# Performance work log

Measured on AMD Instinct MI355X. Metric: run time of the kernel, lower is better.

Reference implementation:

```python
import jax, jax.numpy as jnp
import numpy as np

B, S, E, H = 4, 2048, 256, 8
D = E // H
SCALE = D ** -0.5


def setup_inputs() -> dict:
    key = jax.random.key(0)
    k1, k2, k3, k4, k5, k6 = jax.random.split(key, 6)
    x = jax.random.normal(k1, (B, S, E), dtype=jnp.float32)
    lengths = jax.random.randint(k2, (B,), S // 4, S + 1)
    # binary prefix mask, as assumed by mask[i].sum() == valid length in the original
    mask = (jnp.arange(S)[None, :] < lengths[:, None]).astype(jnp.int32)
    w_std = 1.0 / np.sqrt(E)
    Wq = jax.random.normal(k3, (E, E), dtype=jnp.float32) * w_std
    Wk = jax.random.normal(k4, (E, E), dtype=jnp.float32) * w_std
    Wv = jax.random.normal(k5, (E, E), dtype=jnp.float32) * w_std
    Wo = jax.random.normal(k6, (E, E), dtype=jnp.float32) * w_std
    return {"x": x, "mask": mask, "Wq": Wq, "Wk": Wk, "Wv": Wv, "Wo": Wo}


def _scramble_pad(attn_i, L):
    # attn_i: [S, H, D] attention output for one sample; only query rows < L are used.
    # Faithful to torch: attn[:L] viewed as [H, L, D] (after transpose(1,2)) then
    # reshape(L, E), zero-padded to [S, E]. The reshape mixes heads in a
    # length-dependent way, reproduced here with integer index arithmetic.
    L_safe = jnp.maximum(L, 1)
    flat = jnp.arange(S * E)                     # flat index into [H, L, D] row-major
    h = jnp.minimum(flat // (L_safe * D), H - 1)
    rem = flat % (L_safe * D)
    s = rem // D
    d = rem % D
    valid = flat < L * E
    vals = attn_i[s, h, d]
    return jnp.where(valid, vals, 0.0).reshape(S, E)


def reference(x, mask, Wq, Wk, Wv, Wo):
    # projections (torch Linear, no bias: y = x @ W.T), split heads
    Q = (x @ Wq.T).reshape(B, S, H, D)
    K = (x @ Wk.T).reshape(B, S, H, D)
    V = (x @ Wv.T).reshape(B, S, H, D)
    scores = jnp.einsum("bqhd,bkhd->bhqk", Q, K) * SCALE
    key_valid = mask[:, None, None, :] > 0       # prefix key mask == per-sample varlen attn
    scores = jnp.where(key_valid, scores, -1e30)
    P = jax.nn.softmax(scores, axis=-1)
    attn = jnp.einsum("bhqk,bkhd->bqhd", P, V)   # [B, S, H, D]
    lengths = mask.sum(axis=1)
    padded = jax.vmap(_scramble_pad)(attn, lengths)  # [B, S, E]
    return padded @ Wo.T
```

## Files before the change

### kernel.cpp

```cpp
#include <hip/hip_runtime.h>
#include <cmath>

#define Bn 4
#define Sn 2048
#define En 256
#define Hn 8
#define Dn 32
#define KD 256
#define NS 8
#define CHUNK 256

static constexpr float SCALE_F = 0.17677669529663687f;

typedef _Float16 half4_t __attribute__((ext_vector_type(4)));
typedef _Float16 half8_t __attribute__((ext_vector_type(8)));
typedef float float4_t __attribute__((ext_vector_type(4)));

__global__ __launch_bounds__(256) void len_kernel(const int* __restrict__ mask,
                                                  int* __restrict__ len) {
  int b = blockIdx.x, t = threadIdx.x;
  int s = 0;
  for (int i = t; i < Sn; i += 256) s += mask[b * Sn + i];
#pragma unroll
  for (int off = 32; off > 0; off >>= 1) s += __shfl_down(s, off, 64);
  __shared__ int red[4];
  if ((t & 63) == 0) red[t >> 6] = s;
  __syncthreads();
  if (t == 0) len[b] = red[0] + red[1] + red[2] + red[3];
}

__global__ __launch_bounds__(256) void cvt_kernel(
    const float* __restrict__ x, const float* __restrict__ Wq,
    const float* __restrict__ Wk, const float* __restrict__ Wv,
    const float* __restrict__ Wo, _Float16* __restrict__ xh,
    _Float16* __restrict__ Wh) {
  const size_t base = ((size_t)blockIdx.x * 256 + threadIdx.x) * 8;
  const float* src; _Float16* dst; size_t off;
  if (base < 2097152) { src = x; dst = xh; off = base; }
  else {
    size_t wi = base - 2097152;
    int w = (int)(wi >> 16);
    off = wi & 65535;
    src = (w == 0) ? Wq : (w == 1) ? Wk : (w == 2) ? Wv : Wo;
    dst = Wh + (size_t)w * 65536;
  }
  float4 a = *(const float4*)&src[off];
  float4 b2 = *(const float4*)&src[off + 4];
  half8_t h;
  h[0] = (_Float16)a.x;  h[1] = (_Float16)a.y;
  h[2] = (_Float16)a.z;  h[3] = (_Float16)a.w;
  h[4] = (_Float16)b2.x; h[5] = (_Float16)b2.y;
  h[6] = (_Float16)b2.z; h[7] = (_Float16)b2.w;
  *(half8_t*)&dst[off] = h;
}

__global__ __launch_bounds__(256) void qkv_gemm(
    const _Float16* __restrict__ xh, const _Float16* __restrict__ Wh,
    _Float16* __restrict__ Qh, _Float16* __restrict__ Kh,
    _Float16* __restrict__ Vt) {
  const int lane = threadIdx.x & 63;
  const int wv = threadIdx.x >> 6;
  const int quad = lane >> 4, l15 = lane & 15;
  const int n0 = blockIdx.x * 64;
  const int mw = blockIdx.y * 256 + wv * 64;

  float4_t C[4][4];
#pragma unroll
  for (int i = 0; i < 4; ++i)
#pragma unroll
    for (int j = 0; j < 4; ++j) C[i][j] = (float4_t){0.f, 0.f, 0.f, 0.f};

  for (int k0 = 0; k0 < KD; k0 += 32) {
    half8_t A[4], Bf[4];
#pragma unroll
    for (int i = 0; i < 4; ++i)
      A[i] = *(const half8_t*)&xh[(size_t)(mw + 16 * i + l15) * KD + k0 + quad * 8];
#pragma unroll
    for (int j = 0; j < 4; ++j)
      Bf[j] = *(const half8_t*)&Wh[(size_t)(n0 + 16 * j + l15) * KD + k0 + quad * 8];
#pragma unroll
    for (int i = 0; i < 4; ++i)
#pragma unroll
      for (int j = 0; j < 4; ++j)
        C[i][j] = __builtin_amdgcn_mfma_f32_16x16x32_f16(A[i], Bf[j], C[i][j], 0, 0, 0);
  }

  const int mat = n0 >> 8;
  if (mat < 2) {
    _Float16* dstH = mat ? Kh : Qh;
    const float scale = mat ? 1.0f : SCALE_F;
#pragma unroll
    for (int i = 0; i < 4; ++i)
#pragma unroll
      for (int j = 0; j < 4; ++j) {
        const int c = ((n0 + 16 * j) & 255) + l15;
        const int h = c >> 5, d = c & 31;
#pragma unroll
        for (int r = 0; r < 4; ++r) {
          const int m = mw + 16 * i + quad * 4 + r;
          const int b = m >> 11, s = m & (Sn - 1);
          dstH[((size_t)(b * Hn + h) * Sn + s) * Dn + d] =
              (_Float16)(C[i][j][r] * scale);
        }
      }
  } else {
#pragma unroll
    for (int i = 0; i < 4; ++i)
#pragma unroll
      for (int j = 0; j < 4; ++j) {
        const int c = ((n0 + 16 * j) & 255) + l15;
        const int h = c >> 5, d = c & 31;
        const int m = mw + 16 * i + quad * 4;
        const int b = m >> 11, s = m & (Sn - 1);
        half4_t hv;
#pragma unroll
        for (int r = 0; r < 4; ++r) hv[r] = (_Float16)C[i][j][r];
        *(half4_t*)&Vt[(size_t)(b * Hn + h) * (Sn * Dn) +
                       (size_t)(s >> 5) * 1024 + d * 32 + (s & 31)] = hv;
      }
  }
}

__global__ __launch_bounds__(256) void out_gemm(
    const _Float16* __restrict__ Ph, const _Float16* __restrict__ Woh,
    float* __restrict__ out) {
  const int lane = threadIdx.x & 63;
  const int wv = threadIdx.x >> 6;
  const int quad = lane >> 4, l15 = lane & 15;
  const int n0 = blockIdx.x * 64;
  const int mw = blockIdx.y * 256 + wv * 64;

  float4_t C[4][4];
#pragma unroll
  for (int i = 0; i < 4; ++i)
#pragma unroll
    for (int j = 0; j < 4; ++j) C[i][j] = (float4_t){0.f, 0.f, 0.f, 0.f};

  for (int k0 = 0; k0 < KD; k0 += 32) {
    half8_t A[4], Bf[4];
#pragma unroll
    for (int i = 0; i < 4; ++i)
      A[i] = *(const half8_t*)&Ph[(size_t)(mw + 16 * i + l15) * KD + k0 + quad * 8];
#pragma unroll
    for (int j = 0; j < 4; ++j)
      Bf[j] = *(const half8_t*)&Woh[(size_t)(n0 + 16 * j + l15) * KD + k0 + quad * 8];
#pragma unroll
    for (int i = 0; i < 4; ++i)
#pragma unroll
      for (int j = 0; j < 4; ++j)
        C[i][j] = __builtin_amdgcn_mfma_f32_16x16x32_f16(A[i], Bf[j], C[i][j], 0, 0, 0);
  }

#pragma unroll
  for (int i = 0; i < 4; ++i)
#pragma unroll
    for (int j = 0; j < 4; ++j)
#pragma unroll
      for (int r = 0; r < 4; ++r)
        out[(size_t)(mw + 16 * i + quad * 4 + r) * En + n0 + 16 * j + l15] =
            C[i][j][r];
}

__global__ __launch_bounds__(256) void attn_kernel(
    const _Float16* __restrict__ Qh, const _Float16* __restrict__ Kh,
    const _Float16* __restrict__ Vt, const int* __restrict__ len,
    float* __restrict__ pacc, float* __restrict__ pl) {
  const int split = blockIdx.x & (NS - 1);
  const int qg = blockIdx.x >> 3;
  const int h = blockIdx.y, b = blockIdx.z;
  const int L = len[b];
  const int lane = threadIdx.x & 63;
  const int wv = threadIdx.x >> 6;
  const int q0 = (qg * 4 + wv) * 64;
  if (q0 >= L) return;
  const int ks = split * CHUNK;
  if (ks >= L) return;
  const int ke = min(L, ks + CHUNK);

  const int quad = lane >> 4;
  const int l15 = lane & 15;
  const size_t bh = (size_t)(b * Hn + h) * Sn;
  const _Float16* Vt0 = &Vt[(size_t)(b * Hn + h) * (Sn * Dn)];

  half8_t qf[4];
#pragma unroll
  for (int t = 0; t < 4; ++t)
    qf[t] = *(const half8_t*)&Qh[(bh + q0 + 16 * t + l15) * Dn + quad * 8];

  float4_t o0[4], o1[4];
  float ll[4];
#pragma unroll
  for (int t = 0; t < 4; ++t) {
    o0[t] = (float4_t){0.f, 0.f, 0.f, 0.f};
    o1[t] = (float4_t){0.f, 0.f, 0.f, 0.f};
    ll[t] = 0.f;
  }

  const int vo0 = l15 * 32 + quad * 4;
  const int vo1 = (l15 + 16) * 32 + quad * 4;

  const _Float16* vt_c = &Vt0[(size_t)(ks >> 5) * 1024];
  half8_t kfc0 = *(const half8_t*)&Kh[(bh + ks + l15) * Dn + quad * 8];
  half8_t kfc1 = *(const half8_t*)&Kh[(bh + ks + 16 + l15) * Dn + quad * 8];
  half4_t v0c = *(const half4_t*)&vt_c[vo0];
  half4_t v1c = *(const half4_t*)&vt_c[vo1];
  half4_t v2c = *(const half4_t*)&vt_c[vo0 + 16];
  half4_t v3c = *(const half4_t*)&vt_c[vo1 + 16];

  for (int k0 = ks; k0 < ke; k0 += 32) {
    const int kn = (k0 + 32 < ke) ? k0 + 32 : ks;
    const _Float16* vt_n = &Vt0[(size_t)(kn >> 5) * 1024];
    const half8_t kfn0 = *(const half8_t*)&Kh[(bh + kn + l15) * Dn + quad * 8];
    const half8_t kfn1 = *(const half8_t*)&Kh[(bh + kn + 16 + l15) * Dn + quad * 8];
    const half4_t v0n = *(const half4_t*)&vt_n[vo0];
    const half4_t v1n = *(const half4_t*)&vt_n[vo1];
    const half4_t v2n = *(const half4_t*)&vt_n[vo0 + 16];
    const half4_t v3n = *(const half4_t*)&vt_n[vo1 + 16];

    float4_t st0[4], st1[4];
#pragma unroll
    for (int t = 0; t < 4; ++t) {
      st0[t] = (float4_t){0.f, 0.f, 0.f, 0.f};
      st1[t] = (float4_t){0.f, 0.f, 0.f, 0.f};
      st0[t] = __builtin_amdgcn_mfma_f32_16x16x32_f16(kfc0, qf[t], st0[t], 0, 0, 0);
      st1[t] = __builtin_amdgcn_mfma_f32_16x16x32_f16(kfc1, qf[t], st1[t], 0, 0, 0);
    }
    const int ka = k0 + quad * 4, kb = k0 + 16 + quad * 4;
#pragma unroll
    for (int t = 0; t < 4; ++t) {
      half4_t pf0, pf1;
#pragma unroll
      for (int r = 0; r < 4; ++r) {
        const float pa = __expf((ka + r < ke) ? st0[t][r] : -3.0e38f);
        const float pb = __expf((kb + r < ke) ? st1[t][r] : -3.0e38f);
        ll[t] += pa + pb;
        pf0[r] = (_Float16)pa;
        pf1[r] = (_Float16)pb;
      }
      o0[t] = __builtin_amdgcn_mfma_f32_16x16x16f16(pf0, v0c, o0[t], 0, 0, 0);
      o1[t] = __builtin_amdgcn_mfma_f32_16x16x16f16(pf0, v1c, o1[t], 0, 0, 0);
      o0[t] = __builtin_amdgcn_mfma_f32_16x16x16f16(pf1, v2c, o0[t], 0, 0, 0);
      o1[t] = __builtin_amdgcn_mfma_f32_16x16x16f16(pf1, v3c, o1[t], 0, 0, 0);
    }
    kfc0 = kfn0; kfc1 = kfn1;
    v0c = v0n; v1c = v1n; v2c = v2n; v3c = v3n;
  }

#pragma unroll
  for (int t = 0; t < 4; ++t) {
    ll[t] += __shfl_xor(ll[t], 16);
    ll[t] += __shfl_xor(ll[t], 32);
  }

  const size_t idx0 = ((size_t)(b * Hn + h) * NS + split) * Sn + q0;
#pragma unroll
  for (int t = 0; t < 4; ++t) {
#pragma unroll
    for (int r = 0; r < 4; ++r) {
      float* pp = &pacc[(idx0 + 16 * t + quad * 4 + r) * 32];
      pp[l15] = o0[t][r];
      pp[l15 + 16] = o1[t][r];
    }
  }
  if (quad == 0) {
#pragma unroll
    for (int t = 0; t < 4; ++t) pl[idx0 + 16 * t + l15] = ll[t];
  }
}

__global__ __launch_bounds__(256) void combine_kernel(const float* __restrict__ pacc,
                                                      const float* __restrict__ pl,
                                                      const int* __restrict__ len,
                                                      _Float16* __restrict__ Ph) {
  const int b = blockIdx.z;
  const int L = len[b];
  if (blockIdx.y == Hn) {
    _Float16* base = Ph + (size_t)b * Sn * En;
    const size_t end = (size_t)Sn * En;
    const size_t stride = (size_t)gridDim.x * 256 * 8;
    half8_t z = {0, 0, 0, 0, 0, 0, 0, 0};
    for (size_t idx = (size_t)L * En + ((size_t)blockIdx.x * 256 + threadIdx.x) * 8;
         idx < end; idx += stride)
      *(half8_t*)&base[idx] = z;
    return;
  }
  const int h = blockIdx.y;
  const int q = blockIdx.x * 256 + threadIdx.x;
  if (q >= L) return;
  const size_t base = (size_t)(b * Hn + h) * NS * Sn;

  float T = 0.f;
  float o[32];
#pragma unroll
  for (int d = 0; d < 32; ++d) o[d] = 0.f;
#pragma unroll
  for (int sp = 0; sp < NS; ++sp) {
    if (sp * CHUNK < L) {
      T += pl[base + (size_t)sp * Sn + q];
      const float4* pp = (const float4*)&pacc[(base + (size_t)sp * Sn + q) * 32];
#pragma unroll
      for (int i = 0; i < 8; ++i) {
        float4 v = pp[i];
        o[i * 4 + 0] += v.x;
        o[i * 4 + 1] += v.y;
        o[i * 4 + 2] += v.z;
        o[i * 4 + 3] += v.w;
      }
    }
  }
  const float inv = 1.0f / T;
  _Float16* dst = &Ph[(size_t)b * Sn * En + (size_t)h * L * Dn + (size_t)q * Dn];
#pragma unroll
  for (int i = 0; i < 4; ++i) {
    half8_t hv;
#pragma unroll
    for (int t2 = 0; t2 < 8; ++t2) hv[t2] = (_Float16)(o[i * 8 + t2] * inv);
    *(half8_t*)&dst[i * 8] = hv;
  }
}

extern "C" void kernel_launch(void* const* d_in, const int* in_sizes, int n_in,
                              void* d_out, int out_size, void* d_ws, size_t ws_size,
                              hipStream_t stream) {
  (void)in_sizes; (void)n_in; (void)out_size; (void)ws_size;
  const float* x  = (const float*)d_in[0];
  const int* mask = (const int*)d_in[1];
  const float* Wq = (const float*)d_in[2];
  const float* Wk = (const float*)d_in[3];
  const float* Wv = (const float*)d_in[4];
  const float* Wo = (const float*)d_in[5];
  float* out = (float*)d_out;

  float* wsf = (float*)d_ws;
  int* lengths = (int*)d_ws;
  const size_t BHSD = (size_t)Bn * Hn * Sn * Dn;
  _Float16* xh = (_Float16*)(wsf + 64);
  _Float16* Wh = xh + BHSD;
  _Float16* Qh = Wh + 4 * 65536;
  _Float16* Kh = Qh + BHSD;
  _Float16* Vt = Kh + BHSD;
  _Float16* Ph = Vt + BHSD;
  float* pacc = (float*)(Ph + BHSD);
  float* pl = pacc + (size_t)Bn * Hn * NS * Sn * 32;

  len_kernel<<<dim3(Bn), 256, 0, stream>>>(mask, lengths);
  cvt_kernel<<<dim3((2097152 + 262144) / (256 * 8)), 256, 0, stream>>>(
      x, Wq, Wk, Wv, Wo, xh, Wh);
  qkv_gemm<<<dim3(12, 32), 256, 0, stream>>>(xh, Wh, Qh, Kh, Vt);
  attn_kernel<<<dim3((Sn / 256) * NS, Hn, Bn), 256, 0, stream>>>(
      Qh, Kh, Vt, lengths, pacc, pl);
  combine_kernel<<<dim3(Sn / 256, Hn + 1, Bn), 256, 0, stream>>>(
      pacc, pl, lengths, Ph);
  out_gemm<<<dim3(4, 32), 256, 0, stream>>>(Ph, Wh + 3 * 65536, out);
}
```

Measured before the change: 154.5 us.

## Double KV splits, store fp16 partials, and skip masking on full key tiles

Doubles the number of key splits in the split-K attention, from 8 chunks of 256 keys to 16 chunks of 128, which gives more blocks and less serial work per block. To keep the partial-accumulator traffic bounded, partial outputs are now stored as fp16 instead of fp32, and the combine kernel reads half8 vectors. The softmax loop gets a fast path with no length masking for full 32-key tiles. The costs are twice as many partials to combine and lower precision in the partial sums, since values are unnormalized exps rounded to fp16.

```diff
diff --git a/kernel.cpp b/kernel.cpp
--- a/kernel.cpp
+++ b/kernel.cpp
@@ -7,8 +7,8 @@
 #define Hn 8
 #define Dn 32
 #define KD 256
-#define NS 8
-#define CHUNK 256
+#define NS 16
+#define CHUNK 128
 
 static constexpr float SCALE_F = 0.17677669529663687f;
 
@@ -164,9 +164,9 @@
 __global__ __launch_bounds__(256) void attn_kernel(
     const _Float16* __restrict__ Qh, const _Float16* __restrict__ Kh,
     const _Float16* __restrict__ Vt, const int* __restrict__ len,
-    float* __restrict__ pacc, float* __restrict__ pl) {
+    _Float16* __restrict__ pacc, float* __restrict__ pl) {
   const int split = blockIdx.x & (NS - 1);
-  const int qg = blockIdx.x >> 3;
+  const int qg = blockIdx.x >> 4;
   const int h = blockIdx.y, b = blockIdx.z;
   const int L = len[b];
   const int lane = threadIdx.x & 63;
@@ -225,22 +225,42 @@
       st0[t] = __builtin_amdgcn_mfma_f32_16x16x32_f16(kfc0, qf[t], st0[t], 0, 0, 0);
       st1[t] = __builtin_amdgcn_mfma_f32_16x16x32_f16(kfc1, qf[t], st1[t], 0, 0, 0);
     }
-    const int ka = k0 + quad * 4, kb = k0 + 16 + quad * 4;
-#pragma unroll
-    for (int t = 0; t < 4; ++t) {
-      half4_t pf0, pf1;
-#pragma unroll
-      for (int r = 0; r < 4; ++r) {
-        const float pa = __expf((ka + r < ke) ? st0[t][r] : -3.0e38f);
-        const float pb = __expf((kb + r < ke) ? st1[t][r] : -3.0e38f);
-        ll[t] += pa + pb;
-        pf0[r] = (_Float16)pa;
-        pf1[r] = (_Float16)pb;
-      }
-      o0[t] = __builtin_amdgcn_mfma_f32_16x16x16f16(pf0, v0c, o0[t], 0, 0, 0);
-      o1[t] = __builtin_amdgcn_mfma_f32_16x16x16f16(pf0, v1c, o1[t], 0, 0, 0);
-      o0[t] = __builtin_amdgcn_mfma_f32_16x16x16f16(pf1, v2c, o0[t], 0, 0, 0);
-      o1[t] = __builtin_amdgcn_mfma_f32_16x16x16f16(pf1, v3c, o1[t], 0, 0, 0);
+
+    if (k0 + 32 <= ke) {
+#pragma unroll
+      for (int t = 0; t < 4; ++t) {
+        half4_t pf0, pf1;
+#pragma unroll
+        for (int r = 0; r < 4; ++r) {
+          const float pa = __expf(st0[t][r]);
+          const float pb = __expf(st1[t][r]);
+          ll[t] += pa + pb;
+          pf0[r] = (_Float16)pa;
+          pf1[r] = (_Float16)pb;
+        }
+        o0[t] = __builtin_amdgcn_mfma_f32_16x16x16f16(pf0, v0c, o0[t], 0, 0, 0);
+        o1[t] = __builtin_amdgcn_mfma_f32_16x16x16f16(pf0, v1c, o1[t], 0, 0, 0);
+        o0[t] = __builtin_amdgcn_mfma_f32_16x16x16f16(pf1, v2c, o0[t], 0, 0, 0);
+        o1[t] = __builtin_amdgcn_mfma_f32_16x16x16f16(pf1, v3c, o1[t], 0, 0, 0);
+      }
+    } else {
+      const int ka = k0 + quad * 4, kb = k0 + 16 + quad * 4;
+#pragma unroll
+      for (int t = 0; t < 4; ++t) {
+        half4_t pf0, pf1;
+#pragma unroll
+        for (int r = 0; r < 4; ++r) {
+          const float pa = __expf((ka + r < ke) ? st0[t][r] : -3.0e38f);
+          const float pb = __expf((kb + r < ke) ? st1[t][r] : -3.0e38f);
+          ll[t] += pa + pb;
+          pf0[r] = (_Float16)pa;
+          pf1[r] = (_Float16)pb;
+        }
+        o0[t] = __builtin_amdgcn_mfma_f32_16x16x16f16(pf0, v0c, o0[t], 0, 0, 0);
+        o1[t] = __builtin_amdgcn_mfma_f32_16x16x16f16(pf0, v1c, o1[t], 0, 0, 0);
+        o0[t] = __builtin_amdgcn_mfma_f32_16x16x16f16(pf1, v2c, o0[t], 0, 0, 0);
+        o1[t] = __builtin_amdgcn_mfma_f32_16x16x16f16(pf1, v3c, o1[t], 0, 0, 0);
+      }
     }
     kfc0 = kfn0; kfc1 = kfn1;
     v0c = v0n; v1c = v1n; v2c = v2n; v3c = v3n;
@@ -257,9 +277,9 @@
   for (int t = 0; t < 4; ++t) {
 #pragma unroll
     for (int r = 0; r < 4; ++r) {
-      float* pp = &pacc[(idx0 + 16 * t + quad * 4 + r) * 32];
-      pp[l15] = o0[t][r];
-      pp[l15 + 16] = o1[t][r];
+      _Float16* pp = &pacc[(idx0 + 16 * t + quad * 4 + r) * 32];
+      pp[l15] = (_Float16)o0[t][r];
+      pp[l15 + 16] = (_Float16)o1[t][r];
     }
   }
   if (quad == 0) {
@@ -268,7 +288,7 @@
   }
 }
 
-__global__ __launch_bounds__(256) void combine_kernel(const float* __restrict__ pacc,
+__global__ __launch_bounds__(256) void combine_kernel(const _Float16* __restrict__ pacc,
                                                       const float* __restrict__ pl,
                                                       const int* __restrict__ len,
                                                       _Float16* __restrict__ Ph) {
@@ -297,14 +317,12 @@
   for (int sp = 0; sp < NS; ++sp) {
     if (sp * CHUNK < L) {
       T += pl[base + (size_t)sp * Sn + q];
-      const float4* pp = (const float4*)&pacc[(base + (size_t)sp * Sn + q) * 32];
-#pragma unroll
-      for (int i = 0; i < 8; ++i) {
-        float4 v = pp[i];
-        o[i * 4 + 0] += v.x;
-        o[i * 4 + 1] += v.y;
-        o[i * 4 + 2] += v.z;
-        o[i * 4 + 3] += v.w;
+      const half8_t* pp = (const half8_t*)&pacc[(base + (size_t)sp * Sn + q) * 32];
+#pragma unroll
+      for (int i = 0; i < 4; ++i) {
+        half8_t v = pp[i];
+#pragma unroll
+        for (int t2 = 0; t2 < 8; ++t2) o[i * 8 + t2] += (float)v[t2];
       }
     }
   }
@@ -340,8 +358,8 @@
   _Float16* Kh = Qh + BHSD;
   _Float16* Vt = Kh + BHSD;
   _Float16* Ph = Vt + BHSD;
-  float* pacc = (float*)(Ph + BHSD);
-  float* pl = pacc + (size_t)Bn * Hn * NS * Sn * 32;
+  _Float16* pacc = Ph + BHSD;
+  float* pl = (float*)(pacc + (size_t)Bn * Hn * NS * Sn * 32);
 
   len_kernel<<<dim3(Bn), 256, 0, stream>>>(mask, lengths);
   cvt_kernel<<<dim3((2097152 + 262144) / (256 * 8)), 256, 0, stream>>>(
```

Result: faster. 150.9 us (-2.3%).
